# Performance work log

Measured on AMD Instinct MI355X. Metric: run time of the kernel, lower is better.

## Reference

```python
import jax, jax.numpy as jnp
import numpy as np

C = 192          # channels
HEADS = 4        # num_heads
HID = int(C * 2.66)  # 510, GDFN hidden features
B, H, W = 2, 192, 192


def setup_inputs() -> dict:
    key = jax.random.key(0)
    ks = jax.random.split(key, 8)
    def nrm(k, shape, scale=0.02):
        return jax.random.normal(k, shape, jnp.float32) * scale
    return dict(
        x=jax.random.normal(ks[0], (B, C, H, W), jnp.float32),
        qkv_w=nrm(ks[1], (3 * C, C)),
        qkv_b=jnp.zeros((3 * C,), jnp.float32),
        qkv_dw_w=nrm(ks[2], (3 * C, 1, 3, 3)),
        qkv_dw_b=jnp.zeros((3 * C,), jnp.float32),
        attn_out_w=nrm(ks[3], (C, C)),
        attn_out_b=jnp.zeros((C,), jnp.float32),
        temperature=jnp.ones((HEADS, 1, 1), jnp.float32),
        proj_in_w=nrm(ks[4], (2 * HID, C)),
        proj_in_b=jnp.zeros((2 * HID,), jnp.float32),
        dw_w=nrm(ks[5], (2 * HID, 1, 3, 3)),
        dw_b=jnp.zeros((2 * HID,), jnp.float32),
        proj_out_w=nrm(ks[6], (C, HID)),
        proj_out_b=jnp.zeros((C,), jnp.float32),
    )


def _instance_norm(x):
    # torch InstanceNorm2d default: affine=False, eps=1e-5, biased var over spatial dims
    m = x.mean(axis=(2, 3), keepdims=True)
    v = ((x - m) ** 2).mean(axis=(2, 3), keepdims=True)
    return (x - m) * jax.lax.rsqrt(v + 1e-5)


def _conv1x1(x, w, b):
    return jnp.einsum('oc,bchw->bohw', w, x) + b[None, :, None, None]


def _dwconv3x3(x, w, b):
    y = jax.lax.conv_general_dilated(
        x, w, window_strides=(1, 1), padding='SAME',
        feature_group_count=x.shape[1],
        dimension_numbers=('NCHW', 'OIHW', 'NCHW'))
    return y + b[None, :, None, None]


def _l2norm(x, eps=1e-12):
    # F.normalize(dim=-1)
    n = jnp.sqrt(jnp.sum(x * x, axis=-1, keepdims=True))
    return x / jnp.maximum(n, eps)


def reference(x, qkv_w, qkv_b, qkv_dw_w, qkv_dw_b, attn_out_w, attn_out_b,
              temperature, proj_in_w, proj_in_b, dw_w, dw_b, proj_out_w, proj_out_b):
    b, c, h, w = x.shape
    hw = h * w
    dh = c // HEADS  # per-head channel dim

    # --- transposed (channel) attention branch ---
    y = _instance_norm(x)
    qkv = _dwconv3x3(_conv1x1(y, qkv_w, qkv_b), qkv_dw_w, qkv_dw_b)  # [b, 3c, h, w]
    q, k, v = jnp.split(qkv, 3, axis=1)
    q = _l2norm(q.reshape(b, HEADS, dh, hw))  # normalize along spatial dim
    k = _l2norm(k.reshape(b, HEADS, dh, hw))
    v = v.reshape(b, HEADS, dh, hw)
    attn = jnp.einsum('bhcn,bhdn->bhcd', q, k) * temperature  # small [b,heads,dh,dh]
    attn = jax.nn.softmax(attn, axis=-1)
    out = jnp.einsum('bhcd,bhdn->bhcn', attn, v).reshape(b, c, h, w)
    x = x + _conv1x1(out, attn_out_w, attn_out_b)

    # --- gated depthwise FFN (GDFN) branch ---
    y = _instance_norm(x)
    y = _dwconv3x3(_conv1x1(y, proj_in_w, proj_in_b), dw_w, dw_b)  # [b, 2*HID, h, w]
    y1, y2 = jnp.split(y, 2, axis=1)
    y = _conv1x1(jax.nn.gelu(y1, approximate=False) * y2, proj_out_w, proj_out_b)
    return x + y
```

## Files before the change

kernel.cpp:

```cpp
#include <hip/hip_runtime.h>
#include <math.h>

#define HW 36864
#define IMGW 192

typedef unsigned short u16;
typedef __attribute__((ext_vector_type(8))) short short8;
typedef __attribute__((ext_vector_type(8))) unsigned short ushort8;
typedef __attribute__((ext_vector_type(16))) float f32x16;

__device__ __forceinline__ float b2f(u16 u){ return __uint_as_float(((unsigned)u)<<16); }
__device__ __forceinline__ u16 f2b(float f){
    unsigned u = __float_as_uint(f);
    return (u16)((u + 0x7FFFu + ((u>>16)&1u)) >> 16);
}
__device__ __forceinline__ int perm1020(int m){ return (m&1) ? 510+(m>>1) : (m>>1); }
__device__ __forceinline__ int rot2(int ch){ return ((ch<<2)|(ch>>3)) & 31; }
__device__ __forceinline__ float gelu_exact(float x){
    return 0.5f * x * (1.f + erff(x * 0.70710678118654752f));
}
__device__ __forceinline__ void gll16(const u16* g, u16* l){
    __builtin_amdgcn_global_load_lds(
        (const __attribute__((address_space(1))) void*)g,
        (__attribute__((address_space(3))) void*)l, 16, 0, 0);
}

__global__ __launch_bounds__(256)
void zero_k(float* __restrict__ p, int n)
{
    int i = blockIdx.x * 256 + threadIdx.x;
    if (i < n) p[i] = 0.f;
}

__global__ __launch_bounds__(192)
void prep1_k(const float* __restrict__ w, const float* __restrict__ b,
             const float4* __restrict__ st, u16* __restrict__ wo, float* __restrict__ bo)
{
    int m = blockIdx.x, k = threadIdx.x;
    float4 s = st[k];
    float wv = (m < 576) ? w[(long)m*192 + k] * s.y : 0.f;
    u16 wb = f2b(wv);
    wo[(long)m*192 + k] = wb;
    float contrib = b2f(wb) * s.x;
    for (int off = 32; off; off >>= 1) contrib += __shfl_down(contrib, off);
    __shared__ float red[3];
    if ((k & 63) == 0) red[k >> 6] = contrib;
    __syncthreads();
    if (k == 0) bo[m] = ((m < 576) ? b[m] : 0.f) - (red[0] + red[1] + red[2]);
}

__global__ __launch_bounds__(192)
void prep2_k(const float* __restrict__ w, const float* __restrict__ b,
             const float* __restrict__ s2m, const float* __restrict__ s2r,
             u16* __restrict__ wo, float* __restrict__ bo)
{
    int m = blockIdx.x, k = threadIdx.x;
    bool valid = (m < 1020);
    int src = valid ? perm1020(m) : 0;
    float wv = valid ? w[(long)src*192 + k] * s2r[k] : 0.f;
    u16 wb = f2b(wv);
    wo[(long)m*192 + k] = wb;
    float contrib = b2f(wb) * s2m[k];
    for (int off = 32; off; off >>= 1) contrib += __shfl_down(contrib, off);
    __shared__ float red[3];
    if ((k & 63) == 0) red[k >> 6] = contrib;
    __syncthreads();
    if (k == 0) bo[m] = (valid ? b[src] : 0.f) - (red[0] + red[1] + red[2]);
}

__global__ __launch_bounds__(256)
void prep3_k(const float* __restrict__ w, u16* __restrict__ wo)
{
    int m = blockIdx.x;
    for (int k = threadIdx.x; k < 512; k += 256)
        wo[(long)m*512 + k] = (k < 510) ? f2b(w[(long)m*510 + k]) : (u16)0;
}

__global__ __launch_bounds__(256)
void tn_k(const float* __restrict__ xb, u16* __restrict__ xt,
          float* __restrict__ ps, float* __restrict__ pq)
{
    __shared__ float L[64 * 196];
    long n0 = (long)blockIdx.x * 64;
    int tid = threadIdx.x;
    #pragma unroll
    for (int i = 0; i < 48; ++i) {
        int idx = tid + i*256;
        int n = idx & 63, c = idx >> 6;
        L[n*196 + c] = xb[(long)c*HW + n0 + n];
    }
    __syncthreads();
    if (tid < 192) {
        float s = 0.f, q = 0.f;
        #pragma unroll 8
        for (int n = 0; n < 64; ++n) { float f = L[n*196 + tid]; s += f; q = fmaf(f, f, q); }
        ps[blockIdx.x*192 + tid] = s;
        pq[blockIdx.x*192 + tid] = q;
    }
    #pragma unroll
    for (int i = 0; i < 6; ++i) {
        int idx = tid + i*256;
        int oc = idx % 24, n = idx / 24;
        ushort8 v;
        #pragma unroll
        for (int e = 0; e < 8; ++e) v[e] = f2b(L[n*196 + oc*8 + e]);
        *reinterpret_cast<ushort8*>(xt + (n0+n)*192 + oc*8) = v;
    }
}

__global__ __launch_bounds__(64)
void fin1b_k(const float* __restrict__ ps, const float* __restrict__ pq, float4* __restrict__ st)
{
    int c = blockIdx.x, t = threadIdx.x;
    float s = 0.f, q = 0.f;
    for (int b = t; b < 576; b += 64) { s += ps[b*192 + c]; q += pq[b*192 + c]; }
    for (int off = 32; off; off >>= 1) { s += __shfl_down(s, off); q += __shfl_down(q, off); }
    if (t == 0) {
        float mean = s / (float)HW;
        float var  = q / (float)HW - mean*mean;
        st[c] = make_float4(mean, rsqrtf(var + 1e-5f), 0.f, 0.f);
    }
}

__global__ __launch_bounds__(64)
void fin2b_k(const float* __restrict__ ps, const float* __restrict__ pq,
             float* __restrict__ m, float* __restrict__ r)
{
    int c = blockIdx.x, t = threadIdx.x;
    float s = 0.f, q = 0.f;
    for (int b = t; b < 288; b += 64) { s += ps[b*192 + c]; q += pq[b*192 + c]; }
    for (int off = 32; off; off >>= 1) { s += __shfl_down(s, off); q += __shfl_down(q, off); }
    if (t == 0) {
        float mean = s / (float)HW;
        float var  = q / (float)HW - mean*mean;
        m[c] = mean;
        r[c] = rsqrtf(var + 1e-5f);
    }
}

template<int BM, int RESID, bool OUTT>
__global__ __launch_bounds__(256)
void gemm_k(const u16* __restrict__ W, int Kpad, int K64,
            const u16* __restrict__ B, int brs,
            const float* __restrict__ bias,
            const u16* __restrict__ Rs,
            u16* __restrict__ outA, int ors, int Mout,
            float* __restrict__ outT,
            float* __restrict__ p2s, float* __restrict__ p2q)
{
    constexpr int MR  = BM / 64;
    constexpr int OLS = BM + 8;
    constexpr int L_MAIN = 8192 + BM*64;
    constexpr int L_OUT  = 128*OLS;
    constexpr int LDSU = L_MAIN > L_OUT ? L_MAIN : L_OUT;
    __shared__ u16 lds[LDSU];
    __shared__ float cws[256], cwq[256];
    u16* Xl = lds;
    u16* Wl = lds + 8192;

    const int tid = threadIdx.x;
    const int m0 = blockIdx.x * BM;
    const long nn0 = (long)blockIdx.y * 128;
    const int ln = tid & 63, wv = tid >> 6;
    const int wn = (wv >> 1) * 64;
    const int wm = (wv & 1) * (BM/2);
    const int l31 = ln & 31, l5 = ln >> 5;

    const u16* Bb = B + nn0*(long)brs;
    const u16* Wb = W + (long)m0*Kpad;

    f32x16 acc[2][MR];
    #pragma unroll
    for (int a = 0; a < 2; ++a)
        #pragma unroll
        for (int b = 0; b < MR; ++b)
            #pragma unroll
            for (int r = 0; r < 16; ++r) acc[a][b][r] = 0.f;

    for (int ks = 0; ks < K64; ++ks) {
        #pragma unroll
        for (int i = 0; i < 4; ++i) {
            int chunk = i*256 + tid;
            int row = chunk >> 3, o = chunk & 7;
            int op = o ^ ((row >> 1) & 7);
            gll16(Bb + (long)row*brs + ks*64 + op*8, Xl + chunk*8);
        }
        #pragma unroll
        for (int i = 0; i < BM/32; ++i) {
            int chunk = i*256 + tid;
            int row = chunk >> 3, o = chunk & 7;
            int op = o ^ ((row >> 1) & 7);
            gll16(Wb + (long)row*Kpad + ks*64 + op*8, Wl + chunk*8);
        }
        __syncthreads();
        #pragma unroll
        for (int k16 = 0; k16 < 4; ++k16) {
            short8 af[2];
            #pragma unroll
            for (int nr = 0; nr < 2; ++nr) {
                int row = wn + nr*32 + l31;
                int slot = (k16*2 + l5) ^ ((row >> 1) & 7);
                af[nr] = *reinterpret_cast<const short8*>(&Xl[row*64 + slot*8]);
            }
            short8 bf[MR];
            #pragma unroll
            for (int mr = 0; mr < MR; ++mr) {
                int rowm = wm + mr*32 + l31;
                int slot = (k16*2 + l5) ^ ((rowm >> 1) & 7);
                bf[mr] = *reinterpret_cast<const short8*>(&Wl[rowm*64 + slot*8]);
            }
            #pragma unroll
            for (int nr = 0; nr < 2; ++nr)
                #pragma unroll
                for (int mr = 0; mr < MR; ++mr)
                    acc[nr][mr] = __builtin_amdgcn_mfma_f32_32x32x16_bf16(af[nr], bf[mr], acc[nr][mr], 0, 0, 0);
        }
        __syncthreads();
    }
    float bsv[MR];
    #pragma unroll
    for (int mr = 0; mr < MR; ++mr)
        bsv[mr] = bias[m0 + wm + mr*32 + l31];
    u16* Ol = lds;
    #pragma unroll
    for (int nr = 0; nr < 2; ++nr)
        #pragma unroll
        for (int mr = 0; mr < MR; ++mr)
            #pragma unroll
            for (int reg = 0; reg < 16; ++reg) {
                int r32 = (reg & 3) + 8*(reg >> 2) + 4*l5;
                int grow = wn + nr*32 + r32;
                int gcol = wm + mr*32 + l31;
                float val = acc[nr][mr][reg] + bsv[mr];
                if (RESID == 2)
                    val += b2f(Rs[(nn0 + grow)*192 + m0 + gcol]);
                Ol[grow*OLS + gcol] = f2b(val);
            }
    __syncthreads();
    if (!OUTT) {
        constexpr int SPR = BM/8;
        float ls[8] = {0,0,0,0,0,0,0,0}, lq[8] = {0,0,0,0,0,0,0,0};
        #pragma unroll
        for (int i = 0; i < 128*SPR/256; ++i) {
            int idx = tid + i*256;
            int row = idx / SPR, sl = idx % SPR;
            if (m0 + sl*8 >= Mout) continue;
            ushort8 v = *reinterpret_cast<const ushort8*>(&Ol[row*OLS + sl*8]);
            if (RESID == 1) {
                ushort8 rv = *reinterpret_cast<const ushort8*>(Rs + (nn0+row)*(long)ors + m0 + sl*8);
                #pragma unroll
                for (int e = 0; e < 8; ++e) {
                    v[e] = f2b(b2f(v[e]) + b2f(rv[e]));
                    float vv = b2f(v[e]);
                    ls[e] += vv; lq[e] = fmaf(vv, vv, lq[e]);
                }
            }
            *reinterpret_cast<ushort8*>(outA + (nn0+row)*(long)ors + m0 + sl*8) = v;
        }
        if (RESID == 1) {
            #pragma unroll
            for (int e = 0; e < 8; ++e) {
                float s = ls[e], q = lq[e];
                s += __shfl_xor(s, 8);  q += __shfl_xor(q, 8);
                s += __shfl_xor(s, 16); q += __shfl_xor(q, 16);
                s += __shfl_xor(s, 32); q += __shfl_xor(q, 32);
                if (ln < 8) { cws[wv*64 + ln*8 + e] = s; cwq[wv*64 + ln*8 + e] = q; }
            }
            __syncthreads();
            if (tid < 64) {
                float s = cws[tid] + cws[64+tid] + cws[128+tid] + cws[192+tid];
                float q = cwq[tid] + cwq[64+tid] + cwq[128+tid] + cwq[192+tid];
                p2s[blockIdx.y*192 + m0 + tid] = s;
                p2q[blockIdx.y*192 + m0 + tid] = q;
            }
        }
    } else {
        int m = tid >> 2, ng = tid & 3;
        float* orow = outT + (long)(m0 + m)*HW + nn0 + ng*32;
        #pragma unroll
        for (int i = 0; i < 32; i += 4) {
            float4 o;
            o.x = b2f(Ol[(ng*32+i+0)*OLS + m]);
            o.y = b2f(Ol[(ng*32+i+1)*OLS + m]);
            o.z = b2f(Ol[(ng*32+i+2)*OLS + m]);
            o.w = b2f(Ol[(ng*32+i+3)*OLS + m]);
            *reinterpret_cast<float4*>(orow + i) = o;
        }
    }
}

__global__ __launch_bounds__(256)
void dwconv_k(const u16* __restrict__ in, const float* __restrict__ dww,
              const float* __restrict__ dwb, u16* __restrict__ vbuf,
              u16* __restrict__ qkT, float* __restrict__ nacc, const u16* __restrict__ zp)
{
    __shared__ u16 T[10*34*32];
    __shared__ float wl[32][9];
    __shared__ float bl[32];
    __shared__ float nsum[32];
    const int tid = threadIdx.x;
    const int cg = blockIdx.y;
    const int ty = blockIdx.x / 6, tx = blockIdx.x % 6;
    const int y0 = ty*8, x0 = tx*32;
    const bool isv = (cg >= 12);
    const int cbase = cg*32;

    for (int i = tid; i < 288; i += 256) wl[i/9][i%9] = dww[cbase*9 + i];
    if (tid < 32) { bl[tid] = dwb[cbase + tid]; nsum[tid] = 0.f; }
    #pragma unroll
    for (int it = 0; it < 6; ++it) {
        int i = it*256 + tid;
        if (i < 1360) {
            int r = i / 136;
            int rem = i - r*136;
            int c = rem >> 2, o = rem & 3;
            int gy = y0 - 1 + r, gx = x0 - 1 + c;
            const u16* src = ((unsigned)gy < 192u && (unsigned)gx < 192u)
                ? in + ((long)gy*192 + gx)*576 + cbase + o*8 : zp;
            gll16(src, T + i*8);
        }
    }
    __syncthreads();

    const int o2 = tid & 3, xc = (tid >> 2) & 31, yh = tid >> 7;
    float wr[9][8], bs[8];
    #pragma unroll
    for (int j = 0; j < 9; ++j)
        #pragma unroll
        for (int e = 0; e < 8; ++e) wr[j][e] = wl[o2*8+e][j];
    #pragma unroll
    for (int e = 0; e < 8; ++e) bs[e] = bl[o2*8+e];

    float acc[4][8];
    #pragma unroll
    for (int yy = 0; yy < 4; ++yy)
        #pragma unroll
        for (int e = 0; e < 8; ++e) acc[yy][e] = bs[e];
    #pragma unroll
    for (int r = 0; r < 6; ++r) {
        const int rr = yh*4 + r;
        float f[3][8];
        #pragma unroll
        for (int dx = 0; dx < 3; ++dx) {
            ushort8 v = *reinterpret_cast<const ushort8*>(&T[(rr*34 + xc+dx)*32 + o2*8]);
            #pragma unroll
            for (int e = 0; e < 8; ++e) f[dx][e] = b2f(v[e]);
        }
        #pragma unroll
        for (int yy = 0; yy < 4; ++yy) {
            const int dy = r - yy;
            if (dy < 0 || dy > 2) continue;
            #pragma unroll
            for (int dx = 0; dx < 3; ++dx)
                #pragma unroll
                for (int e = 0; e < 8; ++e)
                    acc[yy][e] = fmaf(f[dx][e], wr[dy*3+dx][e], acc[yy][e]);
        }
    }
    float sq[8] = {0.f,0.f,0.f,0.f,0.f,0.f,0.f,0.f};
    ushort8 ov[4];
    #pragma unroll
    for (int yy = 0; yy < 4; ++yy) {
        int y = yh*4 + yy;
        #pragma unroll
        for (int e = 0; e < 8; ++e) { float a = acc[yy][e]; ov[yy][e] = f2b(a); sq[e] = fmaf(a, a, sq[e]); }
        if (isv)
            *reinterpret_cast<ushort8*>(vbuf + ((long)(y0+y)*192 + x0+xc)*192 + (cg-12)*32 + o2*8) = ov[yy];
    }
    if (!isv) {
        #pragma unroll
        for (int e = 0; e < 8; ++e) {
            float s = sq[e];
            s += __shfl_xor(s, 4); s += __shfl_xor(s, 8);
            s += __shfl_xor(s, 16); s += __shfl_xor(s, 32);
            if ((tid & 63) < 4) atomicAdd(&nsum[o2*8 + e], s);
        }
        __syncthreads();
        if (tid < 32) atomicAdd(&nacc[cbase + tid], nsum[tid]);
        #pragma unroll
        for (int yy = 0; yy < 4; ++yy) {
            int y = yh*4 + yy;
            #pragma unroll
            for (int e = 0; e < 8; ++e) {
                int ch = o2*8 + e;
                int slot = y*4 + (xc >> 3);
                T[ch*256 + ((slot ^ rot2(ch)) & 31)*8 + (xc & 7)] = ov[yy][e];
            }
        }
        __syncthreads();
        #pragma unroll
        for (int i = 0; i < 4; ++i) {
            int idx = i*256 + tid;
            int ch = idx >> 5, slot = idx & 31;
            ushort8 v = *reinterpret_cast<const ushort8*>(&T[ch*256 + ((slot ^ rot2(ch)) & 31)*8]);
            int yy2 = slot >> 2, sx = slot & 3;
            *reinterpret_cast<ushort8*>(qkT + (long)(cbase+ch)*HW + (long)(y0+yy2)*192 + x0 + sx*8) = v;
        }
    }
}

__global__ __launch_bounds__(256)
void attnscore_k(const u16* __restrict__ qkT, float* __restrict__ apart)
{
    __shared__ u16 lds[8192];
    u16* Al = lds;
    u16* Bl = lds + 4096;
    const int tid = threadIdx.x;
    const int h = blockIdx.y;
    const long nb = (long)blockIdx.x * 512;
    const int ln = tid & 63, wv = tid >> 6;
    const int wq = (wv >> 1) * 32, wd = (wv & 1) * 32;
    const int l31 = ln & 31, l5 = ln >> 5;

    f32x16 acc;
    #pragma unroll
    for (int r = 0; r < 16; ++r) acc[r] = 0.f;

    for (int ks = 0; ks < 8; ++ks) {
        #pragma unroll
        for (int i = 0; i < 2; ++i) {
            int chunk = i*256 + tid;
            int row = chunk >> 3, o = chunk & 7;
            int op = o ^ ((row >> 1) & 7);
            int qr = h*48 + (row < 48 ? row : 0);
            gll16(qkT + (long)qr*HW + nb + ks*64 + op*8, Al + chunk*8);
        }
        #pragma unroll
        for (int i = 0; i < 2; ++i) {
            int chunk = i*256 + tid;
            int row = chunk >> 3, o = chunk & 7;
            int op = o ^ ((row >> 1) & 7);
            int kr = 192 + h*48 + (row < 48 ? row : 0);
            gll16(qkT + (long)kr*HW + nb + ks*64 + op*8, Bl + chunk*8);
        }
        __syncthreads();
        #pragma unroll
        for (int k16 = 0; k16 < 4; ++k16) {
            int rq = wq + l31;
            int sq_ = (k16*2 + l5) ^ ((rq >> 1) & 7);
            short8 af = *reinterpret_cast<const short8*>(&Al[rq*64 + sq_*8]);
            int rk = wd + l31;
            int sk = (k16*2 + l5) ^ ((rk >> 1) & 7);
            short8 bf = *reinterpret_cast<const short8*>(&Bl[rk*64 + sk*8]);
            acc = __builtin_amdgcn_mfma_f32_32x32x16_bf16(af, bf, acc, 0, 0, 0);
        }
        __syncthreads();
    }
    float* ap = apart + ((long)blockIdx.x*4 + h) * 2304;
    #pragma unroll
    for (int reg = 0; reg < 16; ++reg) {
        int c = wq + (reg & 3) + 8*(reg >> 2) + 4*l5;
        int d = wd + l31;
        if (c < 48 && d < 48) ap[c*48 + d] = acc[reg];
    }
}

__global__ __launch_bounds__(256)
void red_k(const float* __restrict__ apart, float* __restrict__ araw)
{
    int idx = blockIdx.x*256 + threadIdx.x;
    float s = 0.f;
    for (int p = 0; p < 72; ++p) s += apart[(long)p*9216 + idx];
    araw[idx] = s;
}

__global__ __launch_bounds__(256)
void softmax_sm_k(const float* __restrict__ araw, const float* __restrict__ nacc,
                  const float* __restrict__ temp, float* __restrict__ ssm)
{
    int tid = threadIdx.x;
    if (tid >= 192) return;
    int h = tid / 48, c = tid % 48;
    float qn = fmaxf(sqrtf(nacc[h*48 + c]), 1e-12f);
    float ti = temp[h] / qn;
    const float* ar = araw + h*2304 + c*48;
    const float* nk = nacc + 192 + h*48;
    float row[48];
    float mx = -1e30f;
    #pragma unroll
    for (int d = 0; d < 48; ++d) {
        float kn = fmaxf(sqrtf(nk[d]), 1e-12f);
        row[d] = ar[d] * ti / kn;
        mx = fmaxf(mx, row[d]);
    }
    float ssum = 0.f;
    #pragma unroll
    for (int d = 0; d < 48; ++d) { float e = expf(row[d] - mx); row[d] = e; ssum += e; }
    float inv = 1.f / ssum;
    float* so = ssm + h*2304 + c*48;
    #pragma unroll
    for (int d = 0; d < 48; ++d) so[d] = row[d] * inv;
}

__global__ __launch_bounds__(256)
void w2fold_k(const float* __restrict__ ssm, const float* __restrict__ aow,
              u16* __restrict__ W2b)
{
    int idx = blockIdx.x*256 + threadIdx.x;
    int o = idx / 192, col = idx % 192;
    int h = col / 48, d = col % 48;
    const float* ar = aow + (long)o*192 + h*48;
    const float* sp = ssm + h*2304 + d;
    float s = 0.f;
    #pragma unroll
    for (int c = 0; c < 48; ++c) s = fmaf(ar[c], sp[c*48], s);
    W2b[idx] = f2b(s);
}

__global__ __launch_bounds__(256)
void gate_k(const u16* __restrict__ t2h, const float* __restrict__ dww,
            const float* __restrict__ dwb, u16* __restrict__ g, int jbase,
            const u16* __restrict__ zp)
{
    __shared__ u16 T[10*34*32];
    __shared__ float w1l[16][9], w2l[16][9];
    __shared__ float b1l[16], b2l[16];
    const int tid = threadIdx.x;
    const int cg = blockIdx.y;
    const int ty = blockIdx.x / 6, tx = blockIdx.x % 6;
    const int y0 = ty*8, x0 = tx*32;
    const int jb = jbase + cg*16;

    for (int i = tid; i < 144; i += 256) {
        int p = i/9, j = i%9;
        int gj = jb + p;
        bool ok = (gj < 510);
        w1l[p][j] = ok ? dww[(long)gj*9 + j] : 0.f;
        w2l[p][j] = ok ? dww[(long)(510+gj)*9 + j] : 0.f;
    }
    if (tid < 16) {
        int gj = jb + tid;
        bool ok = (gj < 510);
        b1l[tid] = ok ? dwb[gj] : 0.f;
        b2l[tid] = ok ? dwb[510+gj] : 0.f;
    }
    #pragma unroll
    for (int it = 0; it < 6; ++it) {
        int i = it*256 + tid;
        if (i < 1360) {
            int r = i / 136;
            int rem = i - r*136;
            int c = rem >> 2, o = rem & 3;
            int gy = y0 - 1 + r, gx = x0 - 1 + c;
            const u16* src = ((unsigned)gy < 192u && (unsigned)gx < 192u)
                ? t2h + ((long)gy*192 + gx)*512 + cg*32 + o*8 : zp;
            gll16(src, T + i*8);
        }
    }
    __syncthreads();

    const int o2 = tid & 3, xc = (tid >> 2) & 31, yh = tid >> 7;
    float w1r[4][9], w2r[4][9], b1r[4], b2r[4];
    #pragma unroll
    for (int p = 0; p < 4; ++p) {
        #pragma unroll
        for (int j = 0; j < 9; ++j) { w1r[p][j] = w1l[o2*4+p][j]; w2r[p][j] = w2l[o2*4+p][j]; }
        b1r[p] = b1l[o2*4+p]; b2r[p] = b2l[o2*4+p];
    }
    float a1[4][4], a2[4][4];
    #pragma unroll
    for (int yy = 0; yy < 4; ++yy)
        #pragma unroll
        for (int p = 0; p < 4; ++p) { a1[yy][p] = b1r[p]; a2[yy][p] = b2r[p]; }
    #pragma unroll
    for (int r = 0; r < 6; ++r) {
        const int rr = yh*4 + r;
        float f1[3][4], f2[3][4];
        #pragma unroll
        for (int dx = 0; dx < 3; ++dx) {
            ushort8 v = *reinterpret_cast<const ushort8*>(&T[(rr*34 + xc+dx)*32 + o2*8]);
            #pragma unroll
            for (int p = 0; p < 4; ++p) { f1[dx][p] = b2f(v[2*p]); f2[dx][p] = b2f(v[2*p+1]); }
        }
        #pragma unroll
        for (int yy = 0; yy < 4; ++yy) {
            const int dy = r - yy;
            if (dy < 0 || dy > 2) continue;
            #pragma unroll
            for (int dx = 0; dx < 3; ++dx)
                #pragma unroll
                for (int p = 0; p < 4; ++p) {
                    a1[yy][p] = fmaf(f1[dx][p], w1r[p][dy*3+dx], a1[yy][p]);
                    a2[yy][p] = fmaf(f2[dx][p], w2r[p][dy*3+dx], a2[yy][p]);
                }
        }
    }
    #pragma unroll
    for (int yy = 0; yy < 4; ++yy) {
        int y = yh*4 + yy;
        ushort4 ovv;
        ovv.x = f2b(gelu_exact(a1[yy][0]) * a2[yy][0]);
        ovv.y = f2b(gelu_exact(a1[yy][1]) * a2[yy][1]);
        ovv.z = f2b(gelu_exact(a1[yy][2]) * a2[yy][2]);
        ovv.w = f2b(gelu_exact(a1[yy][3]) * a2[yy][3]);
        *reinterpret_cast<ushort4*>(g + ((long)(y0+y)*192 + x0+xc)*512 + jb + o2*4) = ovv;
    }
}

extern "C" void kernel_launch(void* const* d_in, const int* in_sizes, int n_in,
                              void* d_out, int out_size, void* d_ws, size_t ws_size,
                              hipStream_t stream) {
    const float* x           = (const float*)d_in[0];
    const float* qkv_w       = (const float*)d_in[1];
    const float* qkv_bias    = (const float*)d_in[2];
    const float* qkv_dw_w    = (const float*)d_in[3];
    const float* qkv_dw_b    = (const float*)d_in[4];
    const float* attn_out_w  = (const float*)d_in[5];
    const float* attn_out_b  = (const float*)d_in[6];
    const float* temperature = (const float*)d_in[7];
    const float* proj_in_w   = (const float*)d_in[8];
    const float* proj_in_b   = (const float*)d_in[9];
    const float* dw_w        = (const float*)d_in[10];
    const float* dw_b        = (const float*)d_in[11];
    const float* proj_out_w  = (const float*)d_in[12];
    const float* proj_out_b  = (const float*)d_in[13];
    float* out = (float*)d_out;
    char* ws = (char*)d_ws;

    u16* A_   = (u16*)ws;
    u16* C_   = (u16*)(ws + 14155776);
    u16* vbuf = (u16*)(ws + 14155776 + 42467328);
    u16* qkT  = (u16*)(ws + 14155776 + 42467328 + 14155776);
    u16* E_   = vbuf;
    char* wsm = ws + 99090432;
    u16* W1p = (u16*)(wsm);
    u16* W2p = (u16*)(wsm + 245760);
    u16* W3p = (u16*)(wsm + 245760 + 393216);
    u16* W2b = (u16*)(wsm + 835584);
    float* b1p = (float*)(wsm + 835584 + 73728);
    float* b2p = b1p + 640;
    float* S_  = b2p + 1024;
    float* nacc = S_;
    float* araw = S_ + 384;
    float* ssm  = S_ + 9600;
    float4* st1 = (float4*)(S_ + 18816);
    float* zpadf = S_ + 19584;
    float* s2m  = S_ + 19592;
    float* s2r  = S_ + 19784;
    float* apart = S_ + 19976;
    float* p1s = apart;
    float* p1q = apart + 110592;
    float* p2s = apart;
    float* p2q = apart + 55296;
    const u16* zp = (const u16*)zpadf;

    prep3_k<<<192, 256, 0, stream>>>(proj_out_w, W3p);
    zero_k<<<1, 256, 0, stream>>>(zpadf, 8);

    for (int b = 0; b < 2; ++b) {
        const float* xb = x + (long)b * 192 * HW;
        float* outb = out + (long)b * 192 * HW;

        zero_k<<<2, 256, 0, stream>>>(nacc, 384);
        tn_k<<<576, 256, 0, stream>>>(xb, A_, p1s, p1q);
        fin1b_k<<<192, 64, 0, stream>>>(p1s, p1q, st1);
        prep1_k<<<640, 192, 0, stream>>>(qkv_w, qkv_bias, st1, W1p, b1p);

        gemm_k<128,0,false><<<dim3(5,288), 256, 0, stream>>>(
            W1p, 192, 3, A_, 192, b1p, nullptr, C_, 576, 576, nullptr, nullptr, nullptr);
        dwconv_k<<<dim3(144,18), 256, 0, stream>>>(C_, qkv_dw_w, qkv_dw_b, vbuf, qkT, nacc, zp);
        attnscore_k<<<dim3(72,4), 256, 0, stream>>>(qkT, apart);
        red_k<<<36, 256, 0, stream>>>(apart, araw);
        softmax_sm_k<<<1, 256, 0, stream>>>(araw, nacc, temperature, ssm);
        w2fold_k<<<144, 256, 0, stream>>>(ssm, attn_out_w, W2b);
        gemm_k<64,1,false><<<dim3(3,288), 256, 0, stream>>>(
            W2b, 192, 3, vbuf, 192, attn_out_b, A_, A_, 192, 192, nullptr, p2s, p2q);

        fin2b_k<<<192, 64, 0, stream>>>(p2s, p2q, s2m, s2r);
        prep2_k<<<1024, 192, 0, stream>>>(proj_in_w, proj_in_b, s2m, s2r, W2p, b2p);

        gemm_k<128,0,false><<<dim3(4,288), 256, 0, stream>>>(
            W2p, 192, 3, A_, 192, b2p, nullptr, E_, 512, 512, nullptr, nullptr, nullptr);
        gate_k<<<dim3(144,16), 256, 0, stream>>>(E_, dw_w, dw_b, C_, 0, zp);
        gemm_k<128,0,false><<<dim3(4,288), 256, 0, stream>>>(
            W2p + (long)512*192, 192, 3, A_, 192, b2p + 512, nullptr, E_, 512, 512, nullptr, nullptr, nullptr);
        gate_k<<<dim3(144,16), 256, 0, stream>>>(E_, dw_w, dw_b, C_, 256, zp);

        gemm_k<64,2,true><<<dim3(3,288), 256, 0, stream>>>(
            W3p, 512, 8, C_, 512, proj_out_b, A_, nullptr, 0, 192, outb, nullptr, nullptr);
    }
}
```

Measured before the change: 470.1 us.

## Batch both images into single kernel launches via blockIdx.z when workspace allows

Adds a batch index (blockIdx.z or y) to every kernel and offsets all per-image buffers by it, so each stage runs both images in one launch instead of a host loop of two. This halves the launch count and gives the small kernels (softmax, reductions, prep) and the GEMMs twice the blocks to fill the GPU. It doubles the workspace footprint and falls back to the old per-image loop when the workspace is smaller than the threshold.

```diff
diff --git a/kernel.cpp b/kernel.cpp
--- a/kernel.cpp
+++ b/kernel.cpp
@@ -36,7 +36,8 @@
 void prep1_k(const float* __restrict__ w, const float* __restrict__ b,
              const float4* __restrict__ st, u16* __restrict__ wo, float* __restrict__ bo)
 {
-    int m = blockIdx.x, k = threadIdx.x;
+    int m = blockIdx.x, k = threadIdx.x, bz = blockIdx.y;
+    st += (long)bz*192; wo += (long)bz*640*192; bo += (long)bz*640;
     float4 s = st[k];
     float wv = (m < 576) ? w[(long)m*192 + k] * s.y : 0.f;
     u16 wb = f2b(wv);
@@ -54,7 +55,8 @@
              const float* __restrict__ s2m, const float* __restrict__ s2r,
              u16* __restrict__ wo, float* __restrict__ bo)
 {
-    int m = blockIdx.x, k = threadIdx.x;
+    int m = blockIdx.x, k = threadIdx.x, bz = blockIdx.y;
+    s2m += (long)bz*192; s2r += (long)bz*192; wo += (long)bz*1024*192; bo += (long)bz*1024;
     bool valid = (m < 1020);
     int src = valid ? perm1020(m) : 0;
     float wv = valid ? w[(long)src*192 + k] * s2r[k] : 0.f;
@@ -80,6 +82,9 @@
 void tn_k(const float* __restrict__ xb, u16* __restrict__ xt,
           float* __restrict__ ps, float* __restrict__ pq)
 {
+    const int bz = blockIdx.z;
+    xb += (long)bz*192*HW; xt += (long)bz*HW*192;
+    ps += (long)bz*576*192; pq += (long)bz*576*192;
     __shared__ float L[64 * 196];
     long n0 = (long)blockIdx.x * 64;
     int tid = threadIdx.x;
@@ -111,7 +116,8 @@
 __global__ __launch_bounds__(64)
 void fin1b_k(const float* __restrict__ ps, const float* __restrict__ pq, float4* __restrict__ st)
 {
-    int c = blockIdx.x, t = threadIdx.x;
+    int c = blockIdx.x, t = threadIdx.x, bz = blockIdx.y;
+    ps += (long)bz*576*192; pq += (long)bz*576*192; st += (long)bz*192;
     float s = 0.f, q = 0.f;
     for (int b = t; b < 576; b += 64) { s += ps[b*192 + c]; q += pq[b*192 + c]; }
     for (int off = 32; off; off >>= 1) { s += __shfl_down(s, off); q += __shfl_down(q, off); }
@@ -126,7 +132,8 @@
 void fin2b_k(const float* __restrict__ ps, const float* __restrict__ pq,
              float* __restrict__ m, float* __restrict__ r)
 {
-    int c = blockIdx.x, t = threadIdx.x;
+    int c = blockIdx.x, t = threadIdx.x, bz = blockIdx.y;
+    ps += (long)bz*288*192; pq += (long)bz*288*192; m += (long)bz*192; r += (long)bz*192;
     float s = 0.f, q = 0.f;
     for (int b = t; b < 288; b += 64) { s += ps[b*192 + c]; q += pq[b*192 + c]; }
     for (int off = 32; off; off >>= 1) { s += __shfl_down(s, off); q += __shfl_down(q, off); }
@@ -140,12 +147,12 @@
 
 template<int BM, int RESID, bool OUTT>
 __global__ __launch_bounds__(256)
-void gemm_k(const u16* __restrict__ W, int Kpad, int K64,
-            const u16* __restrict__ B, int brs,
-            const float* __restrict__ bias,
-            const u16* __restrict__ Rs,
-            u16* __restrict__ outA, int ors, int Mout,
-            float* __restrict__ outT,
+void gemm_k(const u16* __restrict__ W, int Kpad, int K64, long wstr,
+            const u16* __restrict__ B, int brs, long bstr,
+            const float* __restrict__ bias, int biasstr,
+            const u16* __restrict__ Rs, long rstr,
+            u16* __restrict__ outA, int ors, long ostr, int Mout,
+            float* __restrict__ outT, long otstr,
             float* __restrict__ p2s, float* __restrict__ p2q)
 {
     constexpr int MR  = BM / 64;
@@ -157,6 +164,11 @@
     __shared__ float cws[256], cwq[256];
     u16* Xl = lds;
     u16* Wl = lds + 8192;
+
+    const int bz = blockIdx.z;
+    W += (long)bz*wstr; B += (long)bz*bstr; bias += (long)bz*biasstr;
+    if (RESID) Rs += (long)bz*rstr;
+    if (!OUTT) outA += (long)bz*ostr; else outT += (long)bz*otstr;
 
     const int tid = threadIdx.x;
     const int m0 = blockIdx.x * BM;
@@ -270,8 +282,8 @@
             if (tid < 64) {
                 float s = cws[tid] + cws[64+tid] + cws[128+tid] + cws[192+tid];
                 float q = cwq[tid] + cwq[64+tid] + cwq[128+tid] + cwq[192+tid];
-                p2s[blockIdx.y*192 + m0 + tid] = s;
-                p2q[blockIdx.y*192 + m0 + tid] = q;
+                p2s[(long)bz*288*192 + blockIdx.y*192 + m0 + tid] = s;
+                p2q[(long)bz*288*192 + blockIdx.y*192 + m0 + tid] = q;
             }
         }
     } else {
@@ -294,6 +306,9 @@
               const float* __restrict__ dwb, u16* __restrict__ vbuf,
               u16* __restrict__ qkT, float* __restrict__ nacc, const u16* __restrict__ zp)
 {
+    const int bz = blockIdx.z;
+    in += (long)bz*HW*576; vbuf += (long)bz*HW*192;
+    qkT += (long)bz*384*HW; nacc += (long)bz*384;
     __shared__ u16 T[10*34*32];
     __shared__ float wl[32][9];
     __shared__ float bl[32];
@@ -402,6 +417,8 @@
 __global__ __launch_bounds__(256)
 void attnscore_k(const u16* __restrict__ qkT, float* __restrict__ apart)
 {
+    const int bz = blockIdx.z;
+    qkT += (long)bz*384*HW; apart += (long)bz*72*9216;
     __shared__ u16 lds[8192];
     u16* Al = lds;
     u16* Bl = lds + 4096;
@@ -458,6 +475,8 @@
 __global__ __launch_bounds__(256)
 void red_k(const float* __restrict__ apart, float* __restrict__ araw)
 {
+    const int bz = blockIdx.y;
+    apart += (long)bz*72*9216; araw += (long)bz*9216;
     int idx = blockIdx.x*256 + threadIdx.x;
     float s = 0.f;
     for (int p = 0; p < 72; ++p) s += apart[(long)p*9216 + idx];
@@ -468,6 +487,8 @@
 void softmax_sm_k(const float* __restrict__ araw, const float* __restrict__ nacc,
                   const float* __restrict__ temp, float* __restrict__ ssm)
 {
+    const int bz = blockIdx.x;
+    araw += (long)bz*9216; nacc += (long)bz*384; ssm += (long)bz*9216;
     int tid = threadIdx.x;
     if (tid >= 192) return;
     int h = tid / 48, c = tid % 48;
@@ -496,6 +517,8 @@
 void w2fold_k(const float* __restrict__ ssm, const float* __restrict__ aow,
               u16* __restrict__ W2b)
 {
+    const int bz = blockIdx.y;
+    ssm += (long)bz*9216; W2b += (long)bz*36864;
     int idx = blockIdx.x*256 + threadIdx.x;
     int o = idx / 192, col = idx % 192;
     int h = col / 48, d = col % 48;
@@ -512,6 +535,8 @@
             const float* __restrict__ dwb, u16* __restrict__ g, int jbase,
             const u16* __restrict__ zp)
 {
+    const int bz = blockIdx.z;
+    t2h += (long)bz*HW*512; g += (long)bz*HW*576;
     __shared__ u16 T[10*34*32];
     __shared__ float w1l[16][9], w2l[16][9];
     __shared__ float b1l[16], b2l[16];
@@ -617,66 +642,108 @@
     float* out = (float*)d_out;
     char* ws = (char*)d_ws;
 
+    const bool batched = (ws_size >= 210000000ull);
+    const long nb = batched ? 2 : 1;
+
+    const long ASZ = (long)HW*192*2;
+    const long CSZ = (long)HW*576*2;
+    const long VSZ = (long)HW*192*2;
+    const long QSZ = (long)384*HW*2;
     u16* A_   = (u16*)ws;
-    u16* C_   = (u16*)(ws + 14155776);
-    u16* vbuf = (u16*)(ws + 14155776 + 42467328);
-    u16* qkT  = (u16*)(ws + 14155776 + 42467328 + 14155776);
+    u16* C_   = (u16*)(ws + nb*ASZ);
+    u16* vbuf = (u16*)(ws + nb*(ASZ + CSZ));
+    u16* qkT  = (u16*)(ws + nb*(ASZ + CSZ + VSZ));
     u16* E_   = vbuf;
-    char* wsm = ws + 99090432;
+    char* wsm = ws + nb*(ASZ + CSZ + VSZ + QSZ);
     u16* W1p = (u16*)(wsm);
-    u16* W2p = (u16*)(wsm + 245760);
-    u16* W3p = (u16*)(wsm + 245760 + 393216);
-    u16* W2b = (u16*)(wsm + 835584);
-    float* b1p = (float*)(wsm + 835584 + 73728);
-    float* b2p = b1p + 640;
-    float* S_  = b2p + 1024;
-    float* nacc = S_;
-    float* araw = S_ + 384;
-    float* ssm  = S_ + 9600;
-    float4* st1 = (float4*)(S_ + 18816);
-    float* zpadf = S_ + 19584;
-    float* s2m  = S_ + 19592;
-    float* s2r  = S_ + 19784;
-    float* apart = S_ + 19976;
+    u16* W2p = (u16*)(wsm + nb*245760);
+    u16* W3p = (u16*)(wsm + nb*(245760 + 393216));
+    u16* W2b = (u16*)(wsm + nb*(245760 + 393216) + 196608);
+    float* b1p = (float*)(wsm + nb*(245760 + 393216 + 73728) + 196608);
+    float* b2p = b1p + nb*640;
+    float* S_  = b2p + nb*1024;
+    float* zpadf = S_;
+    float* nacc  = S_ + 8;
+    float* araw  = nacc + nb*384;
+    float* ssm   = araw + nb*9216;
+    float4* st1  = (float4*)(ssm + nb*9216);
+    float* s2m   = (float*)(st1 + nb*192);
+    float* s2r   = s2m + nb*192;
+    float* apart = s2r + nb*192;
     float* p1s = apart;
-    float* p1q = apart + 110592;
+    float* p1q = apart + nb*110592;
     float* p2s = apart;
-    float* p2q = apart + 55296;
+    float* p2q = apart + nb*55296;
     const u16* zp = (const u16*)zpadf;
 
+    const long AE = (long)HW*192;
+    const long CE = (long)HW*576;
+    const long VE = (long)HW*192;
+    const long QE = (long)384*HW;
+    const long EE = (long)HW*512;
+
     prep3_k<<<192, 256, 0, stream>>>(proj_out_w, W3p);
-    zero_k<<<1, 256, 0, stream>>>(zpadf, 8);
-
-    for (int b = 0; b < 2; ++b) {
-        const float* xb = x + (long)b * 192 * HW;
-        float* outb = out + (long)b * 192 * HW;
-
-        zero_k<<<2, 256, 0, stream>>>(nacc, 384);
-        tn_k<<<576, 256, 0, stream>>>(xb, A_, p1s, p1q);
-        fin1b_k<<<192, 64, 0, stream>>>(p1s, p1q, st1);
-        prep1_k<<<640, 192, 0, stream>>>(qkv_w, qkv_bias, st1, W1p, b1p);
-
-        gemm_k<128,0,false><<<dim3(5,288), 256, 0, stream>>>(
-            W1p, 192, 3, A_, 192, b1p, nullptr, C_, 576, 576, nullptr, nullptr, nullptr);
-        dwconv_k<<<dim3(144,18), 256, 0, stream>>>(C_, qkv_dw_w, qkv_dw_b, vbuf, qkT, nacc, zp);
-        attnscore_k<<<dim3(72,4), 256, 0, stream>>>(qkT, apart);
-        red_k<<<36, 256, 0, stream>>>(apart, araw);
-        softmax_sm_k<<<1, 256, 0, stream>>>(araw, nacc, temperature, ssm);
-        w2fold_k<<<144, 256, 0, stream>>>(ssm, attn_out_w, W2b);
-        gemm_k<64,1,false><<<dim3(3,288), 256, 0, stream>>>(
-            W2b, 192, 3, vbuf, 192, attn_out_b, A_, A_, 192, 192, nullptr, p2s, p2q);
-
-        fin2b_k<<<192, 64, 0, stream>>>(p2s, p2q, s2m, s2r);
-        prep2_k<<<1024, 192, 0, stream>>>(proj_in_w, proj_in_b, s2m, s2r, W2p, b2p);
-
-        gemm_k<128,0,false><<<dim3(4,288), 256, 0, stream>>>(
-            W2p, 192, 3, A_, 192, b2p, nullptr, E_, 512, 512, nullptr, nullptr, nullptr);
-        gate_k<<<dim3(144,16), 256, 0, stream>>>(E_, dw_w, dw_b, C_, 0, zp);
-        gemm_k<128,0,false><<<dim3(4,288), 256, 0, stream>>>(
-            W2p + (long)512*192, 192, 3, A_, 192, b2p + 512, nullptr, E_, 512, 512, nullptr, nullptr, nullptr);
-        gate_k<<<dim3(144,16), 256, 0, stream>>>(E_, dw_w, dw_b, C_, 256, zp);
-
-        gemm_k<64,2,true><<<dim3(3,288), 256, 0, stream>>>(
-            W3p, 512, 8, C_, 512, proj_out_b, A_, nullptr, 0, 192, outb, nullptr, nullptr);
-    }
-}
+
+    if (batched) {
+        zero_k<<<4, 256, 0, stream>>>(S_, 8 + 2*384);
+        tn_k<<<dim3(576,1,2), 256, 0, stream>>>(x, A_, p1s, p1q);
+        fin1b_k<<<dim3(192,2), 64, 0, stream>>>(p1s, p1q, st1);
+        prep1_k<<<dim3(640,2), 192, 0, stream>>>(qkv_w, qkv_bias, st1, W1p, b1p);
+
+        gemm_k<128,0,false><<<dim3(5,288,2), 256, 0, stream>>>(
+            W1p, 192, 3, 640*192, A_, 192, AE, b1p, 640, nullptr, 0, C_, 576, CE, 576, nullptr, 0, nullptr, nullptr);
+        dwconv_k<<<dim3(144,18,2), 256, 0, stream>>>(C_, qkv_dw_w, qkv_dw_b, vbuf, qkT, nacc, zp);
+        attnscore_k<<<dim3(72,4,2), 256, 0, stream>>>(qkT, apart);
+        red_k<<<dim3(36,2), 256, 0, stream>>>(apart, araw);
+        softmax_sm_k<<<2, 256, 0, stream>>>(araw, nacc, temperature, ssm);
+        w2fold_k<<<dim3(144,2), 256, 0, stream>>>(ssm, attn_out_w, W2b);
+        gemm_k<64,1,false><<<dim3(3,288,2), 256, 0, stream>>>(
+            W2b, 192, 3, 36864, vbuf, 192, VE, attn_out_b, 0, A_, AE, A_, 192, AE, 192, nullptr, 0, p2s, p2q);
+
+        fin2b_k<<<dim3(192,2), 64, 0, stream>>>(p2s, p2q, s2m, s2r);
+        prep2_k<<<dim3(1024,2), 192, 0, stream>>>(proj_in_w, proj_in_b, s2m, s2r, W2p, b2p);
+
+        gemm_k<128,0,false><<<dim3(4,288,2), 256, 0, stream>>>(
+            W2p, 192, 3, 1024*192, A_, 192, AE, b2p, 1024, nullptr, 0, E_, 512, EE, 512, nullptr, 0, nullptr, nullptr);
+        gate_k<<<dim3(144,16,2), 256, 0, stream>>>(E_, dw_w, dw_b, C_, 0, zp);
+        gemm_k<128,0,false><<<dim3(4,288,2), 256, 0, stream>>>(
+            W2p + (long)512*192, 192, 3, 1024*192, A_, 192, AE, b2p + 512, 1024, nullptr, 0, E_, 512, EE, 512, nullptr, 0, nullptr, nullptr);
+        gate_k<<<dim3(144,16,2), 256, 0, stream>>>(E_, dw_w, dw_b, C_, 256, zp);
+
+        gemm_k<64,2,true><<<dim3(3,288,2), 256, 0, stream>>>(
+            W3p, 512, 8, 0, C_, 512, CE, proj_out_b, 0, A_, AE, nullptr, 0, 0, 192, out, (long)192*HW, nullptr, nullptr);
+    } else {
+        for (int b = 0; b < 2; ++b) {
+            const float* xb = x + (long)b * 192 * HW;
+            float* outb = out + (long)b * 192 * HW;
+
+            zero_k<<<2, 256, 0, stream>>>(S_, 8 + 384);
+            tn_k<<<dim3(576,1,1), 256, 0, stream>>>(xb, A_, p1s, p1q);
+            fin1b_k<<<dim3(192,1), 64, 0, stream>>>(p1s, p1q, st1);
+            prep1_k<<<dim3(640,1), 192, 0, stream>>>(qkv_w, qkv_bias, st1, W1p, b1p);
+
+            gemm_k<128,0,false><<<dim3(5,288,1), 256, 0, stream>>>(
+                W1p, 192, 3, 0, A_, 192, 0, b1p, 0, nullptr, 0, C_, 576, 0, 576, nullptr, 0, nullptr, nullptr);
+            dwconv_k<<<dim3(144,18,1), 256, 0, stream>>>(C_, qkv_dw_w, qkv_dw_b, vbuf, qkT, nacc, zp);
+            attnscore_k<<<dim3(72,4,1), 256, 0, stream>>>(qkT, apart);
+            red_k<<<dim3(36,1), 256, 0, stream>>>(apart, araw);
+            softmax_sm_k<<<1, 256, 0, stream>>>(araw, nacc, temperature, ssm);
+            w2fold_k<<<dim3(144,1), 256, 0, stream>>>(ssm, attn_out_w, W2b);
+            gemm_k<64,1,false><<<dim3(3,288,1), 256, 0, stream>>>(
+                W2b, 192, 3, 0, vbuf, 192, 0, attn_out_b, 0, A_, 0, A_, 192, 0, 192, nullptr, 0, p2s, p2q);
+
+            fin2b_k<<<dim3(192,1), 64, 0, stream>>>(p2s, p2q, s2m, s2r);
+            prep2_k<<<dim3(1024,1), 192, 0, stream>>>(proj_in_w, proj_in_b, s2m, s2r, W2p, b2p);
+
+            gemm_k<128,0,false><<<dim3(4,288,1), 256, 0, stream>>>(
+                W2p, 192, 3, 0, A_, 192, 0, b2p, 0, nullptr, 0, E_, 512, 0, 512, nullptr, 0, nullptr, nullptr);
+            gate_k<<<dim3(144,16,1), 256, 0, stream>>>(E_, dw_w, dw_b, C_, 0, zp);
+            gemm_k<128,0,false><<<dim3(4,288,1), 256, 0, stream>>>(
+                W2p + (long)512*192, 192, 3, 0, A_, 192, 0, b2p + 512, 0, nullptr, 0, E_, 512, 0, 512, nullptr, 0, nullptr, nullptr);
+            gate_k<<<dim3(144,16,1), 256, 0, stream>>>(E_, dw_w, dw_b, C_, 256, zp);
+
+            gemm_k<64,2,true><<<dim3(3,288,1), 256, 0, stream>>>(
+                W3p, 512, 8, 0, C_, 512, 0, proj_out_b, 0, A_, 0, nullptr, 0, 0, 192, outb, 0, nullptr, nullptr);
+        }
+    }
+}
```

Measured after the change: 395.9 us. 15.8% less time.
